# Kernel optimization log

Measured on AMD Instinct MI355X. Metric: run time of the kernel, lower is better.

Reference implementation:

```python
import jax, jax.numpy as jnp
import numpy as np

B, N, F = 32, 64, 128

def mish(x):
    return x * jnp.tanh(jax.nn.softplus(x))

def residual_mlp(x, W1, b1, W2, b2):
    # ResidualModule(simple_mlp(d, d, d)): x + Linear2(mish(Linear1(x)))
    h = mish(x @ W1 + b1)
    return x + (h @ W2 + b2)

def setup_inputs() -> dict:
    key = jax.random.key(0)
    ks = jax.random.split(key, 20)
    inp = {
        'embeddings': jax.random.normal(ks[0], (B * N, F), dtype=jnp.float32),
        'num_objects': jnp.full((B,), N, dtype=jnp.int64 if jax.config.jax_enable_x64 else jnp.int32),
    }
    i = 1
    # arity-1 predicate p0: width F; arity-2 predicates p1..p3: width 2F
    for name, d in [('p0', F), ('p1', 2 * F), ('p2', 2 * F), ('p3', 2 * F)]:
        inp[f'W1_{name}'] = jax.random.normal(ks[i], (d, d), dtype=jnp.float32) * 0.05; i += 1
        inp[f'b1_{name}'] = jnp.zeros((d,), dtype=jnp.float32)
        inp[f'W2_{name}'] = jax.random.normal(ks[i], (d, d), dtype=jnp.float32) * 0.05; i += 1
        inp[f'b2_{name}'] = jnp.zeros((d,), dtype=jnp.float32)
    return inp

def reference(embeddings, num_objects,
              W1_p0, b1_p0, W2_p0, b2_p0,
              W1_p1, b1_p1, W2_p1, b2_p1,
              W1_p2, b1_p2, W2_p2, b2_p2,
              W1_p3, b1_p3, W2_p3, b2_p3):
    b = num_objects.shape[0]
    n = embeddings.shape[0] // b          # uniform object count per state
    f = embeddings.shape[1]
    x = embeddings.reshape(b, n, f)       # per-state object embeddings
    # arity 1: every object is a length-1 permutation -> rows are embeddings themselves
    rows_a1 = embeddings                  # [b*n, f]
    # arity 2: all ordered pairs (product with replacement) -> concat features
    left = jnp.broadcast_to(x[:, :, None, :], (b, n, n, f))
    right = jnp.broadcast_to(x[:, None, :, :], (b, n, n, f))
    rows_a2 = jnp.concatenate([left, right], axis=-1).reshape(b * n * n, 2 * f)
    out_p0 = residual_mlp(rows_a1, W1_p0, b1_p0, W2_p0, b2_p0)
    out_p1 = residual_mlp(rows_a2, W1_p1, b1_p1, W2_p1, b2_p1)
    out_p2 = residual_mlp(rows_a2, W1_p2, b1_p2, W2_p2, b2_p2)
    out_p3 = residual_mlp(rows_a2, W1_p3, b1_p3, W2_p3, b2_p3)
    return (out_p0, out_p1, out_p2, out_p3)
```

## Files before the change

kernel.cpp:

```cpp
#include <hip/hip_runtime.h>

typedef __bf16 bf16;
typedef bf16 bf16x8 __attribute__((ext_vector_type(8)));
typedef bf16 bf16x4 __attribute__((ext_vector_type(4)));
typedef float floatx4 __attribute__((ext_vector_type(4)));

__device__ __forceinline__ float mish_f(float x) {
  float e = __expf(fminf(x, 20.0f));
  float p = 1.0f + e;
  float p2 = p * p;
  return x * (p2 - 1.0f) * __builtin_amdgcn_rcpf(p2 + 1.0f);
}

struct PrepArgs {
  const float* emb;
  const float* W[8];
  bf16* emb_bf;
  bf16* Wp[8];
};

__global__ __launch_bounds__(256) void prep_kernel(PrepArgs a) {
  const int idx = blockIdx.x * 256 + threadIdx.x;
  const int EMB_N = 2048 * 128;
  if (idx < EMB_N) {
    a.emb_bf[idx] = (bf16)a.emb[idx];
    return;
  }
  int t = idx - EMB_N;
  int m, local, D, lognct;
  if (t < 32768) {
    m = t >> 14; local = t & 16383; D = 128; lognct = 3;
  } else {
    int u = t - 32768;
    m = 2 + (u >> 16); local = u & 65535; D = 256; lognct = 4;
  }
  if (m >= 8) return;
  const int j    = local & 7;
  const int lane = (local >> 3) & 63;
  const int ctk  = local >> 9;
  const int ct   = ctk & ((1 << lognct) - 1);
  const int kt   = ctk >> lognct;
  const int row  = kt * 32 + (lane >> 4) * 8 + j;
  const int col  = ct * 16 + (lane & 15);
  a.Wp[m][local] = (bf16)a.W[m][row * D + col];
}

template <int NCT, int NKT, int STRIDE, int CPW>
__device__ __forceinline__ void gemm_tiles(const bf16* lds_a,
                                           const bf16* __restrict__ Wp,
                                           int w, int lane,
                                           floatx4 acc[4][CPW]) {
  const int l15 = lane & 15;
  const int q   = lane >> 4;
  for (int kt = 0; kt < NKT; ++kt) {
    bf16x8 af[4];
#pragma unroll
    for (int mt = 0; mt < 4; ++mt)
      af[mt] = *(const bf16x8*)&lds_a[(mt * 16 + l15) * STRIDE + kt * 32 + q * 8];
    bf16x8 bfr[CPW];
#pragma unroll
    for (int c = 0; c < CPW; ++c)
      bfr[c] = *(const bf16x8*)(Wp + (((kt * NCT) + (w * CPW + c)) * 64 + lane) * 8);
#pragma unroll
    for (int mt = 0; mt < 4; ++mt)
#pragma unroll
      for (int c = 0; c < CPW; ++c)
        acc[mt][c] = __builtin_amdgcn_mfma_f32_16x16x32_bf16(af[mt], bfr[c], acc[mt][c], 0, 0, 0);
  }
}

struct UVArgs {
  const bf16* emb_bf;
  const bf16* W1p[3];
  const float* b1[3];
  float* U[3];
  float* V[3];
};

__global__ __launch_bounds__(256) void uv_kernel(UVArgs a) {
  const int p  = blockIdx.y;
  const int r0 = blockIdx.x * 64;
  const int t  = threadIdx.x;
  const int lane = t & 63;
  const int w    = t >> 6;
  const int l15  = lane & 15;
  const int q    = lane >> 4;

  __shared__ bf16 lds[64 * 136];

  {
    const int row = t >> 2;
    const int qt  = t & 3;
    const uint4* s4 = (const uint4*)(a.emb_bf + (r0 + row) * 128 + qt * 32);
    uint4* d4 = (uint4*)&lds[row * 136 + qt * 32];
#pragma unroll
    for (int u = 0; u < 4; ++u) d4[u] = s4[u];
  }
  __syncthreads();

  floatx4 acc[4][4];

#pragma unroll
  for (int mt = 0; mt < 4; ++mt)
#pragma unroll
    for (int c = 0; c < 4; ++c) acc[mt][c] = (floatx4){0.f, 0.f, 0.f, 0.f};
  gemm_tiles<16, 4, 136, 4>(lds, a.W1p[p], w, lane, acc);

  float b1v[4];
#pragma unroll
  for (int c = 0; c < 4; ++c) b1v[c] = a.b1[p][w * 64 + c * 16 + l15];

  float* Up = a.U[p] + (size_t)r0 * 256;
#pragma unroll
  for (int mt = 0; mt < 4; ++mt)
#pragma unroll
    for (int c = 0; c < 4; ++c) {
      const int col = w * 64 + c * 16 + l15;
#pragma unroll
      for (int r = 0; r < 4; ++r) {
        const int rl = mt * 16 + q * 4 + r;
        Up[rl * 256 + col] = acc[mt][c][r] + b1v[c];
      }
    }

#pragma unroll
  for (int mt = 0; mt < 4; ++mt)
#pragma unroll
    for (int c = 0; c < 4; ++c) acc[mt][c] = (floatx4){0.f, 0.f, 0.f, 0.f};
  gemm_tiles<16, 4, 136, 4>(lds, a.W1p[p] + 32768, w, lane, acc);

  float* Vp = a.V[p] + (size_t)r0 * 256;
#pragma unroll
  for (int mt = 0; mt < 4; ++mt)
#pragma unroll
    for (int c = 0; c < 4; ++c) {
      const int col = w * 64 + c * 16 + l15;
#pragma unroll
      for (int r = 0; r < 4; ++r) {
        const int rl = mt * 16 + q * 4 + r;
        Vp[rl * 256 + col] = acc[mt][c][r];
      }
    }
}

struct A2Args {
  const float* U[3];
  const float* V[3];
  const float* emb_f;
  const bf16* W2p[3];
  const float* b2[3];
  float* out[3];
};

__global__ __launch_bounds__(256, 4) void fused_a2(A2Args a) {
  const int p  = blockIdx.y;
  const int r0 = blockIdx.x * 64;
  const int bb = r0 >> 12;
  const int ii = (r0 >> 6) & 63;
  const int t  = threadIdx.x;
  const int lane = t & 63;
  const int w    = t >> 6;
  const int l15  = lane & 15;
  const int q    = lane >> 4;

  __shared__ bf16 lds[64 * 264];

  {
    const int col4 = t & 63;
    const int wq   = t >> 6;
    const floatx4 uvv =
        ((const floatx4*)(a.U[p] + (size_t)(bb * 64 + ii) * 256))[col4];
    const float* Vblk = a.V[p] + (size_t)(bb * 64) * 256;
#pragma unroll
    for (int r = 0; r < 16; ++r) {
      const int row = wq * 16 + r;
      const floatx4 v = ((const floatx4*)(Vblk + row * 256))[col4];
      bf16x4 hv;
#pragma unroll
      for (int e = 0; e < 4; ++e) hv[e] = (bf16)mish_f(uvv[e] + v[e]);
      *(bf16x4*)&lds[row * 264 + col4 * 4] = hv;
    }
  }
  __syncthreads();

  floatx4 acc[4][4];
#pragma unroll
  for (int mt = 0; mt < 4; ++mt)
#pragma unroll
    for (int c = 0; c < 4; ++c) acc[mt][c] = (floatx4){0.f, 0.f, 0.f, 0.f};
  gemm_tiles<16, 8, 264, 4>(lds, a.W2p[p], w, lane, acc);

  float b2v[4];
  {
    const float* b2 = a.b2[p];
#pragma unroll
    for (int c = 0; c < 4; ++c) b2v[c] = b2[w * 64 + c * 16 + l15];
  }
  const float* embL = a.emb_f + (size_t)(bb * 64 + ii) * 128;
  const float* embR = a.emb_f + (size_t)(bb * 64) * 128;
  float* outp = a.out[p] + (size_t)r0 * 256;

  if (w < 2) {
    float resv[4];
#pragma unroll
    for (int c = 0; c < 4; ++c) resv[c] = embL[w * 64 + c * 16 + l15];
#pragma unroll
    for (int mt = 0; mt < 4; ++mt)
#pragma unroll
      for (int c = 0; c < 4; ++c) {
        const int col = w * 64 + c * 16 + l15;
#pragma unroll
        for (int r = 0; r < 4; ++r) {
          const int rl = mt * 16 + q * 4 + r;
          __builtin_nontemporal_store(acc[mt][c][r] + b2v[c] + resv[c],
                                      &outp[rl * 256 + col]);
        }
      }
  } else {
#pragma unroll
    for (int mt = 0; mt < 4; ++mt)
#pragma unroll
      for (int c = 0; c < 4; ++c) {
        const int col = w * 64 + c * 16 + l15;
#pragma unroll
        for (int r = 0; r < 4; ++r) {
          const int rl = mt * 16 + q * 4 + r;
          __builtin_nontemporal_store(
              acc[mt][c][r] + b2v[c] + embR[rl * 128 + (col - 128)],
              &outp[rl * 256 + col]);
        }
      }
  }
}

struct A1Args {
  const bf16* emb_bf;
  const float* emb_f;
  const bf16* W1p;
  const float* b1;
  const bf16* W2p;
  const float* b2;
  float* out;
};

__global__ __launch_bounds__(256, 4) void fused_a1(A1Args a) {
  const int r0 = blockIdx.x * 64;
  const int t  = threadIdx.x;
  const int lane = t & 63;
  const int w    = t >> 6;
  const int l15  = lane & 15;
  const int q    = lane >> 4;

  __shared__ bf16 lds[64 * 136];

  {
    const int row = t >> 2;
    const int qt  = t & 3;
    const bf16* src = a.emb_bf + (r0 + row) * 128 + qt * 32;
    const uint4* s4 = (const uint4*)src;
    uint4* d4 = (uint4*)&lds[row * 136 + qt * 32];
#pragma unroll
    for (int u = 0; u < 4; ++u) d4[u] = s4[u];
  }
  __syncthreads();

  floatx4 acc[4][2];
#pragma unroll
  for (int mt = 0; mt < 4; ++mt)
#pragma unroll
    for (int c = 0; c < 2; ++c) acc[mt][c] = (floatx4){0.f, 0.f, 0.f, 0.f};
  gemm_tiles<8, 4, 136, 2>(lds, a.W1p, w, lane, acc);

  float b1v[2];
#pragma unroll
  for (int c = 0; c < 2; ++c) b1v[c] = a.b1[w * 32 + c * 16 + l15];

  __syncthreads();
#pragma unroll
  for (int mt = 0; mt < 4; ++mt)
#pragma unroll
    for (int c = 0; c < 2; ++c) {
      const int col = w * 32 + c * 16 + l15;
#pragma unroll
      for (int r = 0; r < 4; ++r) {
        float x = acc[mt][c][r] + b1v[c];
        lds[(mt * 16 + q * 4 + r) * 136 + col] = (bf16)mish_f(x);
      }
    }
  __syncthreads();

#pragma unroll
  for (int mt = 0; mt < 4; ++mt)
#pragma unroll
    for (int c = 0; c < 2; ++c) acc[mt][c] = (floatx4){0.f, 0.f, 0.f, 0.f};
  gemm_tiles<8, 4, 136, 2>(lds, a.W2p, w, lane, acc);

  float b2v[2];
#pragma unroll
  for (int c = 0; c < 2; ++c) b2v[c] = a.b2[w * 32 + c * 16 + l15];

#pragma unroll
  for (int mt = 0; mt < 4; ++mt)
#pragma unroll
    for (int c = 0; c < 2; ++c) {
      const int col = w * 32 + c * 16 + l15;
#pragma unroll
      for (int r = 0; r < 4; ++r) {
        const int rl = mt * 16 + q * 4 + r;
        a.out[(r0 + rl) * 128 + col] =
            acc[mt][c][r] + b2v[c] + a.emb_f[(r0 + rl) * 128 + col];
      }
    }
}

extern "C" void kernel_launch(void* const* d_in, const int* in_sizes, int n_in,
                              void* d_out, int out_size, void* d_ws, size_t ws_size,
                              hipStream_t stream) {
  const float* emb_f = (const float*)d_in[0];
  const float* W1s[4], *b1s[4], *W2s[4], *b2s[4];
  for (int p = 0; p < 4; ++p) {
    W1s[p] = (const float*)d_in[2 + p * 4 + 0];
    b1s[p] = (const float*)d_in[2 + p * 4 + 1];
    W2s[p] = (const float*)d_in[2 + p * 4 + 2];
    b2s[p] = (const float*)d_in[2 + p * 4 + 3];
  }

  char* ws = (char*)d_ws;
  bf16* emb_bf = (bf16*)ws;
  size_t off = (size_t)2048 * 128 * 2;
  bf16* Wp[8];
  const size_t wbytes[8] = {32768, 32768, 131072, 131072, 131072, 131072, 131072, 131072};
  for (int m = 0; m < 8; ++m) { Wp[m] = (bf16*)(ws + off); off += wbytes[m]; }
  float* Ub[3];
  float* Vb[3];
  for (int p = 0; p < 3; ++p) {
    Ub[p] = (float*)(ws + off) + (size_t)p * 2 * 2048 * 256;
    Vb[p] = Ub[p] + (size_t)2048 * 256;
  }

  PrepArgs pa;
  pa.emb = emb_f;
  pa.emb_bf = emb_bf;
  const float* Wsrc[8] = {W1s[0], W2s[0], W1s[1], W2s[1], W1s[2], W2s[2], W1s[3], W2s[3]};
  for (int m = 0; m < 8; ++m) { pa.W[m] = Wsrc[m]; pa.Wp[m] = Wp[m]; }
  prep_kernel<<<2688, 256, 0, stream>>>(pa);

  UVArgs uva;
  uva.emb_bf = emb_bf;
  for (int p = 0; p < 3; ++p) {
    uva.W1p[p] = Wp[2 + p * 2];
    uva.b1[p]  = b1s[p + 1];
    uva.U[p]   = Ub[p];
    uva.V[p]   = Vb[p];
  }
  uv_kernel<<<dim3(32, 3), 256, 0, stream>>>(uva);

  float* out = (float*)d_out;

  A1Args a1;
  a1.emb_bf = emb_bf; a1.emb_f = emb_f;
  a1.W1p = Wp[0]; a1.b1 = b1s[0]; a1.W2p = Wp[1]; a1.b2 = b2s[0];
  a1.out = out;
  fused_a1<<<32, 256, 0, stream>>>(a1);

  A2Args a2;
  a2.emb_f = emb_f;
  size_t o = 2048 * 128;
  for (int p = 0; p < 3; ++p) {
    a2.U[p] = Ub[p];
    a2.V[p] = Vb[p];
    a2.W2p[p] = Wp[3 + p * 2];
    a2.b2[p] = b2s[p + 1];
    a2.out[p] = out + o + (size_t)p * 131072 * 256;
  }
  fused_a2<<<dim3(2048, 3), 256, 0, stream>>>(a2);
}
```

Measured before the change: 508.5 us.

## Make fused_a2 persistent with double-buffered LDS and XCD-aware tile assignment

Replaces the 6144-block grid with 512 persistent blocks of 512 threads. Each block loops over 12 row tiles, assigned so consecutive blocks on the same XCD share a contiguous range. U/V loads for the next tile are issued before the current GEMM, and mish for the next tile is written into a second LDS buffer after the stores, so global loads, the mish math and the MFMA work overlap. The GEMM runs at raised wave priority. In exchange it doubles LDS use, spreads columns across 8 waves (2 column tiles each), and keeps prefetched registers live, which may reduce occupancy.

```diff
diff --git a/kernel.cpp b/kernel.cpp
--- a/kernel.cpp
+++ b/kernel.cpp
@@ -152,84 +152,109 @@
   float* out[3];
 };
 
-__global__ __launch_bounds__(256, 4) void fused_a2(A2Args a) {
-  const int p  = blockIdx.y;
-  const int r0 = blockIdx.x * 64;
-  const int bb = r0 >> 12;
-  const int ii = (r0 >> 6) & 63;
-  const int t  = threadIdx.x;
+__global__ __launch_bounds__(512, 4) void fused_a2(A2Args a) {
+  const int t    = threadIdx.x;
   const int lane = t & 63;
   const int w    = t >> 6;
   const int l15  = lane & 15;
   const int q    = lane >> 4;
-
-  __shared__ bf16 lds[64 * 264];
-
-  {
-    const int col4 = t & 63;
-    const int wq   = t >> 6;
-    const floatx4 uvv =
-        ((const floatx4*)(a.U[p] + (size_t)(bb * 64 + ii) * 256))[col4];
-    const float* Vblk = a.V[p] + (size_t)(bb * 64) * 256;
-#pragma unroll
-    for (int r = 0; r < 16; ++r) {
-      const int row = wq * 16 + r;
-      const floatx4 v = ((const floatx4*)(Vblk + row * 256))[col4];
+  const int col4 = t & 63;
+  const int rg   = t >> 6;
+
+  __shared__ bf16 lds[2][64 * 264];
+
+  const int xcd   = blockIdx.x & 7;
+  const int slot  = blockIdx.x >> 3;
+  const int tbase = xcd * 768 + slot * 12;
+
+  floatx4 vv[8];
+  floatx4 uq;
+
+  auto load_uv = [&](int tf) {
+    const int pp = tf >> 11;
+    const int rr = tf & 2047;
+    const int bb = rr >> 6, ii = rr & 63;
+    uq = ((const floatx4*)(a.U[pp] + (size_t)(bb * 64 + ii) * 256))[col4];
+    const float* Vblk = a.V[pp] + (size_t)(bb * 64 + rg * 8) * 256;
+#pragma unroll
+    for (int r = 0; r < 8; ++r)
+      vv[r] = ((const floatx4*)(Vblk + (size_t)r * 256))[col4];
+  };
+  auto mish_write = [&](bf16* buf) {
+#pragma unroll
+    for (int r = 0; r < 8; ++r) {
       bf16x4 hv;
 #pragma unroll
-      for (int e = 0; e < 4; ++e) hv[e] = (bf16)mish_f(uvv[e] + v[e]);
-      *(bf16x4*)&lds[row * 264 + col4 * 4] = hv;
-    }
-  }
+      for (int e = 0; e < 4; ++e) hv[e] = (bf16)mish_f(uq[e] + vv[r][e]);
+      *(bf16x4*)&buf[(rg * 8 + r) * 264 + col4 * 4] = hv;
+    }
+  };
+
+  load_uv(tbase);
+  mish_write(&lds[0][0]);
   __syncthreads();
 
-  floatx4 acc[4][4];
-#pragma unroll
-  for (int mt = 0; mt < 4; ++mt)
-#pragma unroll
-    for (int c = 0; c < 4; ++c) acc[mt][c] = (floatx4){0.f, 0.f, 0.f, 0.f};
-  gemm_tiles<16, 8, 264, 4>(lds, a.W2p[p], w, lane, acc);
-
-  float b2v[4];
-  {
-    const float* b2 = a.b2[p];
-#pragma unroll
-    for (int c = 0; c < 4; ++c) b2v[c] = b2[w * 64 + c * 16 + l15];
-  }
-  const float* embL = a.emb_f + (size_t)(bb * 64 + ii) * 128;
-  const float* embR = a.emb_f + (size_t)(bb * 64) * 128;
-  float* outp = a.out[p] + (size_t)r0 * 256;
-
-  if (w < 2) {
-    float resv[4];
-#pragma unroll
-    for (int c = 0; c < 4; ++c) resv[c] = embL[w * 64 + c * 16 + l15];
+  for (int it = 0; it < 12; ++it) {
+    const int ct    = tbase + it;
+    const int cpred = ct >> 11;
+    const int crem  = ct & 2047;
+    const int cbb   = crem >> 6;
+    const int cii   = crem & 63;
+    const bf16* curb = &lds[it & 1][0];
+    bf16* nxtb       = &lds[(it & 1) ^ 1][0];
+
+    if (it + 1 < 12) load_uv(ct + 1);
+
+    floatx4 acc[4][2];
 #pragma unroll
     for (int mt = 0; mt < 4; ++mt)
 #pragma unroll
-      for (int c = 0; c < 4; ++c) {
-        const int col = w * 64 + c * 16 + l15;
-#pragma unroll
-        for (int r = 0; r < 4; ++r) {
-          const int rl = mt * 16 + q * 4 + r;
-          __builtin_nontemporal_store(acc[mt][c][r] + b2v[c] + resv[c],
-                                      &outp[rl * 256 + col]);
+      for (int c = 0; c < 2; ++c) acc[mt][c] = (floatx4){0.f, 0.f, 0.f, 0.f};
+    __builtin_amdgcn_s_setprio(1);
+    gemm_tiles<16, 8, 264, 2>(curb, a.W2p[cpred], w, lane, acc);
+    __builtin_amdgcn_s_setprio(0);
+
+    float b2v[2];
+#pragma unroll
+    for (int c = 0; c < 2; ++c) b2v[c] = a.b2[cpred][w * 32 + c * 16 + l15];
+    const float* embL = a.emb_f + (size_t)(cbb * 64 + cii) * 128;
+    const float* embR = a.emb_f + (size_t)(cbb * 64) * 128;
+    float* outp = a.out[cpred] + (size_t)crem * 64 * 256;
+
+    if (w < 4) {
+      float resv[2];
+#pragma unroll
+      for (int c = 0; c < 2; ++c) resv[c] = embL[w * 32 + c * 16 + l15];
+#pragma unroll
+      for (int mt = 0; mt < 4; ++mt)
+#pragma unroll
+        for (int c = 0; c < 2; ++c) {
+          const int col = w * 32 + c * 16 + l15;
+#pragma unroll
+          for (int r = 0; r < 4; ++r) {
+            const int rl = mt * 16 + q * 4 + r;
+            __builtin_nontemporal_store(acc[mt][c][r] + b2v[c] + resv[c],
+                                        &outp[rl * 256 + col]);
+          }
         }
-      }
-  } else {
-#pragma unroll
-    for (int mt = 0; mt < 4; ++mt)
-#pragma unroll
-      for (int c = 0; c < 4; ++c) {
-        const int col = w * 64 + c * 16 + l15;
-#pragma unroll
-        for (int r = 0; r < 4; ++r) {
-          const int rl = mt * 16 + q * 4 + r;
-          __builtin_nontemporal_store(
-              acc[mt][c][r] + b2v[c] + embR[rl * 128 + (col - 128)],
-              &outp[rl * 256 + col]);
+    } else {
+#pragma unroll
+      for (int mt = 0; mt < 4; ++mt)
+#pragma unroll
+        for (int c = 0; c < 2; ++c) {
+          const int col = w * 32 + c * 16 + l15;
+#pragma unroll
+          for (int r = 0; r < 4; ++r) {
+            const int rl = mt * 16 + q * 4 + r;
+            __builtin_nontemporal_store(
+                acc[mt][c][r] + b2v[c] + embR[rl * 128 + (col - 128)],
+                &outp[rl * 256 + col]);
+          }
         }
-      }
+    }
+
+    if (it + 1 < 12) mish_write(nxtb);
+    __syncthreads();
   }
 }
 
@@ -373,5 +398,5 @@
     a2.b2[p] = b2s[p + 1];
     a2.out[p] = out + o + (size_t)p * 131072 * 256;
   }
-  fused_a2<<<dim3(2048, 3), 256, 0, stream>>>(a2);
-}
+  fused_a2<<<512, 512, 0, stream>>>(a2);
+}
```

After: 677.9 us. +33.3%, slower.
